# Performance work log

Measured on AMD Instinct MI355X. Metric: run time of the kernel, lower is better.

Reference implementation:

```python
import jax, jax.numpy as jnp
import numpy as np


def setup_inputs() -> dict:
    key = jax.random.key(0)
    B, C, H, W = 64, 128, 64, 64
    x = jax.random.normal(key, (B, C, H, W), dtype=jnp.float32)
    return {"x": x}


def reference(x) -> jnp.ndarray:
    # Covariance pooling: y = x_flat @ I_hat @ x_flat^T with
    # I_hat = (1/M) I - (1/M^2) ones(M,M).
    # Algebraically identical to (1/M) * (x - mean)(x - mean)^T, which
    # avoids materializing the MxM centering matrix.
    B, C, H, W = x.shape
    M = H * W
    xf = x.reshape(B, C, M)
    xc = xf - jnp.mean(xf, axis=2, keepdims=True)  # center over spatial dim
    y = jnp.einsum('bcm,bdm->bcd', xc, xc) / M     # [B, C, C]
    return y
```

## Files before the change

kernel.cpp:

```cpp
#include <hip/hip_runtime.h>

typedef __bf16 bf16x8 __attribute__((ext_vector_type(8)));
typedef float  f32x4  __attribute__((ext_vector_type(4)));
typedef unsigned short us8 __attribute__((ext_vector_type(8)));

#define B_      64
#define C_      128
#define M_      4096
#define KCHUNK  8
#define KC      (M_ / KCHUNK)
#define BK      64
#define NSLAB   (KC / BK)
#define LSTR    72

__device__ __forceinline__ unsigned short f2bf(float f) {
  unsigned u = __builtin_bit_cast(unsigned, f);
  u += 0x7fffu + ((u >> 16) & 1u);
  return (unsigned short)(u >> 16);
}
__device__ __forceinline__ float bf2f(unsigned short h) {
  unsigned u = ((unsigned)h) << 16;
  return __builtin_bit_cast(float, u);
}

__global__ __launch_bounds__(512, 4) void covpool_main(
    const float* __restrict__ x, unsigned short* __restrict__ Gp, float* __restrict__ Sp) {
  __shared__ unsigned short As[2][C_ * LSTR];

  const int tid  = threadIdx.x;
  const int b    = blockIdx.x >> 3;
  const int ch   = blockIdx.x & 7;

  const int row  = tid >> 3;
  const int col8 = tid & 7;

  const float* xp0 = x + ((size_t)(b * C_ + row) * M_) + (size_t)ch * KC + col8 * 8;
  const float* xp1 = xp0 + (size_t)64 * M_;

  const int lane = tid & 63;
  const int wave = tid >> 6;
  const int row0 = (wave >> 2) << 6;
  const int col0 = (wave & 3) << 5;
  const int lrow = lane & 15;
  const int quad = lane >> 4;

  f32x4 acc[4][2];
#pragma unroll
  for (int i = 0; i < 4; ++i)
#pragma unroll
    for (int j = 0; j < 2; ++j)
      acc[i][j] = (f32x4){0.f, 0.f, 0.f, 0.f};

  float sum0 = 0.f, sum1 = 0.f;

  float4 r0, r1, r2, r3;
  r0 = ((const float4*)xp0)[0]; r1 = ((const float4*)xp0)[1];
  r2 = ((const float4*)xp1)[0]; r3 = ((const float4*)xp1)[1];

#define STAGE(BUF)                                                                  \
  {                                                                                 \
    sum0 += (r0.x + r0.y) + (r0.z + r0.w) + (r1.x + r1.y) + (r1.z + r1.w);          \
    sum1 += (r2.x + r2.y) + (r2.z + r2.w) + (r3.x + r3.y) + (r3.z + r3.w);          \
    us8 v0 = { f2bf(r0.x), f2bf(r0.y), f2bf(r0.z), f2bf(r0.w),                      \
               f2bf(r1.x), f2bf(r1.y), f2bf(r1.z), f2bf(r1.w) };                    \
    us8 v1 = { f2bf(r2.x), f2bf(r2.y), f2bf(r2.z), f2bf(r2.w),                      \
               f2bf(r3.x), f2bf(r3.y), f2bf(r3.z), f2bf(r3.w) };                    \
    *(__shared__ us8*)&As[BUF][row * LSTR + col8 * 8]        = v0;                  \
    *(__shared__ us8*)&As[BUF][(64 + row) * LSTR + col8 * 8] = v1;                  \
  }

#define COMPUTE(BUF)                                                                \
  {                                                                                 \
    _Pragma("unroll")                                                               \
    for (int ks = 0; ks < 2; ++ks) {                                                \
      const int koff = ks * 32 + quad * 8;                                          \
      bf16x8 af[4], bfr[2];                                                         \
      _Pragma("unroll")                                                             \
      for (int i = 0; i < 4; ++i)                                                   \
        af[i] = *(const __shared__ bf16x8*)&As[BUF][(row0 + i * 16 + lrow) * LSTR + koff]; \
      _Pragma("unroll")                                                             \
      for (int j = 0; j < 2; ++j)                                                   \
        bfr[j] = *(const __shared__ bf16x8*)&As[BUF][(col0 + j * 16 + lrow) * LSTR + koff]; \
      _Pragma("unroll")                                                             \
      for (int i = 0; i < 4; ++i)                                                   \
        _Pragma("unroll")                                                           \
        for (int j = 0; j < 2; ++j)                                                 \
          acc[i][j] = __builtin_amdgcn_mfma_f32_16x16x32_bf16(af[i], bfr[j], acc[i][j], 0, 0, 0); \
    }                                                                               \
  }

#pragma unroll
  for (int s = 0; s < NSLAB; ++s) {
    STAGE(s & 1);
    __syncthreads();
    if (s + 1 < NSLAB) {
      const float* p0 = xp0 + (size_t)(s + 1) * BK;
      const float* p1 = xp1 + (size_t)(s + 1) * BK;
      r0 = ((const float4*)p0)[0]; r1 = ((const float4*)p0)[1];
      r2 = ((const float4*)p1)[0]; r3 = ((const float4*)p1)[1];
    }
    COMPUTE(s & 1);
  }

  unsigned short* gout = Gp + (((size_t)ch * B_ + b) << 14);
#pragma unroll
  for (int i = 0; i < 4; ++i)
#pragma unroll
    for (int j = 0; j < 2; ++j)
#pragma unroll
      for (int rr = 0; rr < 4; ++rr)
        gout[(size_t)(row0 + i * 16 + quad * 4 + rr) * C_ + (col0 + j * 16 + lrow)] =
            f2bf(acc[i][j][rr]);

  sum0 += __shfl_xor(sum0, 1); sum0 += __shfl_xor(sum0, 2); sum0 += __shfl_xor(sum0, 4);
  sum1 += __shfl_xor(sum1, 1); sum1 += __shfl_xor(sum1, 2); sum1 += __shfl_xor(sum1, 4);
  if ((tid & 7) == 0) {
    float* sout = Sp + (((size_t)ch * B_ + b) << 7);
    sout[row]      = sum0;
    sout[64 + row] = sum1;
  }
}

__global__ __launch_bounds__(256) void covpool_fix(
    const unsigned short* __restrict__ Gp, const float* __restrict__ Sp,
    float* __restrict__ y) {
  const int idx = (blockIdx.x * 256 + threadIdx.x) * 4;
  const int bb  = idx >> 14;
  const int rem = idx & 16383;
  const int cc  = rem >> 7;
  const int dd  = rem & 127;
  float g0 = 0.f, g1 = 0.f, g2 = 0.f, g3 = 0.f, sc = 0.f;
  float4 sd = {0.f, 0.f, 0.f, 0.f};
#pragma unroll
  for (int ch = 0; ch < KCHUNK; ++ch) {
    ushort4 gv = *(const ushort4*)&Gp[(((size_t)ch * B_ + bb) << 14) + rem];
    g0 += bf2f(gv.x); g1 += bf2f(gv.y); g2 += bf2f(gv.z); g3 += bf2f(gv.w);
    const float* sp = Sp + (((size_t)ch * B_ + bb) << 7);
    sc += sp[cc];
    float4 s4 = *(const float4*)&sp[dd];
    sd.x += s4.x; sd.y += s4.y; sd.z += s4.z; sd.w += s4.w;
  }
  const float invM = 1.f / (float)M_;
  const float scm = sc * invM;
  float4 out = { g0 * invM - scm * (sd.x * invM), g1 * invM - scm * (sd.y * invM),
                 g2 * invM - scm * (sd.z * invM), g3 * invM - scm * (sd.w * invM) };
  *(float4*)&y[idx] = out;
}

extern "C" void kernel_launch(void* const* d_in, const int* in_sizes, int n_in,
                              void* d_out, int out_size, void* d_ws, size_t ws_size,
                              hipStream_t stream) {
  const float* x = (const float*)d_in[0];
  float* out = (float*)d_out;
  unsigned short* wsG = (unsigned short*)d_ws;
  float* wsS = (float*)(wsG + (size_t)KCHUNK * B_ * C_ * C_);
  covpool_main<<<dim3(B_ * KCHUNK), dim3(512), 0, stream>>>(x, wsG, wsS);
  covpool_fix<<<dim3((B_ * C_ * C_) / 1024), dim3(256), 0, stream>>>(wsG, wsS, out);
}
```

Before: 197.1 us.

## Use larger single-buffered K slabs with batched per-row float4 loads

```diff
diff --git a/kernel.cpp b/kernel.cpp
--- a/kernel.cpp
+++ b/kernel.cpp
@@ -2,21 +2,20 @@
 
 typedef __bf16 bf16x8 __attribute__((ext_vector_type(8)));
 typedef float  f32x4  __attribute__((ext_vector_type(4)));
-typedef unsigned short us8 __attribute__((ext_vector_type(8)));
+typedef unsigned short us4 __attribute__((ext_vector_type(4)));
 
 #define B_      64
 #define C_      128
 #define M_      4096
 #define KCHUNK  8
 #define KC      (M_ / KCHUNK)
-#define BK      64
+#define BK      256
 #define NSLAB   (KC / BK)
-#define LSTR    72
+#define LSTR    264
 
 __device__ __forceinline__ unsigned short f2bf(float f) {
   unsigned u = __builtin_bit_cast(unsigned, f);
-  u += 0x7fffu + ((u >> 16) & 1u);
-  return (unsigned short)(u >> 16);
+  return (unsigned short)((u + 0x8000u) >> 16);
 }
 __device__ __forceinline__ float bf2f(unsigned short h) {
   unsigned u = ((unsigned)h) << 16;
@@ -25,20 +24,20 @@
 
 __global__ __launch_bounds__(512, 4) void covpool_main(
     const float* __restrict__ x, unsigned short* __restrict__ Gp, float* __restrict__ Sp) {
-  __shared__ unsigned short As[2][C_ * LSTR];
+  __shared__ unsigned short As[C_ * LSTR];
 
   const int tid  = threadIdx.x;
   const int b    = blockIdx.x >> 3;
   const int ch   = blockIdx.x & 7;
 
-  const int row  = tid >> 3;
-  const int col8 = tid & 7;
-
-  const float* xp0 = x + ((size_t)(b * C_ + row) * M_) + (size_t)ch * KC + col8 * 8;
-  const float* xp1 = xp0 + (size_t)64 * M_;
-
   const int lane = tid & 63;
   const int wave = tid >> 6;
+
+  const int lr   = lane >> 2;
+  const int q    = lane & 3;
+  const int row  = wave * 16 + lr;
+  const float* rowbase = x + ((size_t)(b * C_ + row) * M_) + (size_t)ch * KC;
+
   const int row0 = (wave >> 2) << 6;
   const int col0 = (wave & 3) << 5;
   const int lrow = lane & 15;
@@ -51,55 +50,48 @@
     for (int j = 0; j < 2; ++j)
       acc[i][j] = (f32x4){0.f, 0.f, 0.f, 0.f};
 
-  float sum0 = 0.f, sum1 = 0.f;
-
-  float4 r0, r1, r2, r3;
-  r0 = ((const float4*)xp0)[0]; r1 = ((const float4*)xp0)[1];
-  r2 = ((const float4*)xp1)[0]; r3 = ((const float4*)xp1)[1];
-
-#define STAGE(BUF)                                                                  \
-  {                                                                                 \
-    sum0 += (r0.x + r0.y) + (r0.z + r0.w) + (r1.x + r1.y) + (r1.z + r1.w);          \
-    sum1 += (r2.x + r2.y) + (r2.z + r2.w) + (r3.x + r3.y) + (r3.z + r3.w);          \
-    us8 v0 = { f2bf(r0.x), f2bf(r0.y), f2bf(r0.z), f2bf(r0.w),                      \
-               f2bf(r1.x), f2bf(r1.y), f2bf(r1.z), f2bf(r1.w) };                    \
-    us8 v1 = { f2bf(r2.x), f2bf(r2.y), f2bf(r2.z), f2bf(r2.w),                      \
-               f2bf(r3.x), f2bf(r3.y), f2bf(r3.z), f2bf(r3.w) };                    \
-    *(__shared__ us8*)&As[BUF][row * LSTR + col8 * 8]        = v0;                  \
-    *(__shared__ us8*)&As[BUF][(64 + row) * LSTR + col8 * 8] = v1;                  \
-  }
-
-#define COMPUTE(BUF)                                                                \
-  {                                                                                 \
-    _Pragma("unroll")                                                               \
-    for (int ks = 0; ks < 2; ++ks) {                                                \
-      const int koff = ks * 32 + quad * 8;                                          \
-      bf16x8 af[4], bfr[2];                                                         \
-      _Pragma("unroll")                                                             \
-      for (int i = 0; i < 4; ++i)                                                   \
-        af[i] = *(const __shared__ bf16x8*)&As[BUF][(row0 + i * 16 + lrow) * LSTR + koff]; \
-      _Pragma("unroll")                                                             \
-      for (int j = 0; j < 2; ++j)                                                   \
-        bfr[j] = *(const __shared__ bf16x8*)&As[BUF][(col0 + j * 16 + lrow) * LSTR + koff]; \
-      _Pragma("unroll")                                                             \
-      for (int i = 0; i < 4; ++i)                                                   \
-        _Pragma("unroll")                                                           \
-        for (int j = 0; j < 2; ++j)                                                 \
-          acc[i][j] = __builtin_amdgcn_mfma_f32_16x16x32_bf16(af[i], bfr[j], acc[i][j], 0, 0, 0); \
-    }                                                                               \
-  }
+  float sum = 0.f;
 
 #pragma unroll
   for (int s = 0; s < NSLAB; ++s) {
-    STAGE(s & 1);
+    const float4* rp = (const float4*)(rowbase + s * BK);
+    float4 L[8];
+#pragma unroll
+    for (int jj = 0; jj < 8; ++jj) L[jj] = rp[q + 4 * jj];
+#pragma unroll
+    for (int jj = 0; jj < 8; ++jj) {
+      float4 v = L[jj];
+      sum += (v.x + v.y) + (v.z + v.w);
+      us4 h = { f2bf(v.x), f2bf(v.y), f2bf(v.z), f2bf(v.w) };
+      *(__shared__ us4*)&As[row * LSTR + (q + 4 * jj) * 4] = h;
+    }
+#pragma unroll
+    for (int jj = 0; jj < 8; ++jj) L[jj] = rp[q + 4 * (8 + jj)];
+#pragma unroll
+    for (int jj = 0; jj < 8; ++jj) {
+      float4 v = L[jj];
+      sum += (v.x + v.y) + (v.z + v.w);
+      us4 h = { f2bf(v.x), f2bf(v.y), f2bf(v.z), f2bf(v.w) };
+      *(__shared__ us4*)&As[row * LSTR + (q + 4 * (8 + jj)) * 4] = h;
+    }
     __syncthreads();
-    if (s + 1 < NSLAB) {
-      const float* p0 = xp0 + (size_t)(s + 1) * BK;
-      const float* p1 = xp1 + (size_t)(s + 1) * BK;
-      r0 = ((const float4*)p0)[0]; r1 = ((const float4*)p0)[1];
-      r2 = ((const float4*)p1)[0]; r3 = ((const float4*)p1)[1];
+#pragma unroll
+    for (int ks = 0; ks < 8; ++ks) {
+      const int koff = ks * 32 + quad * 8;
+      bf16x8 af[4], bfr[2];
+#pragma unroll
+      for (int i = 0; i < 4; ++i)
+        af[i] = *(const __shared__ bf16x8*)&As[(row0 + i * 16 + lrow) * LSTR + koff];
+#pragma unroll
+      for (int j = 0; j < 2; ++j)
+        bfr[j] = *(const __shared__ bf16x8*)&As[(col0 + j * 16 + lrow) * LSTR + koff];
+#pragma unroll
+      for (int i = 0; i < 4; ++i)
+#pragma unroll
+        for (int j = 0; j < 2; ++j)
+          acc[i][j] = __builtin_amdgcn_mfma_f32_16x16x32_bf16(af[i], bfr[j], acc[i][j], 0, 0, 0);
     }
-    COMPUTE(s & 1);
+    __syncthreads();
   }
 
   unsigned short* gout = Gp + (((size_t)ch * B_ + b) << 14);
@@ -112,12 +104,10 @@
         gout[(size_t)(row0 + i * 16 + quad * 4 + rr) * C_ + (col0 + j * 16 + lrow)] =
             f2bf(acc[i][j][rr]);
 
-  sum0 += __shfl_xor(sum0, 1); sum0 += __shfl_xor(sum0, 2); sum0 += __shfl_xor(sum0, 4);
-  sum1 += __shfl_xor(sum1, 1); sum1 += __shfl_xor(sum1, 2); sum1 += __shfl_xor(sum1, 4);
-  if ((tid & 7) == 0) {
+  sum += __shfl_xor(sum, 1); sum += __shfl_xor(sum, 2);
+  if (q == 0) {
     float* sout = Sp + (((size_t)ch * B_ + b) << 7);
-    sout[row]      = sum0;
-    sout[64 + row] = sum1;
+    sout[row] = sum;
   }
 }
 
```

Result: no change. 199.8 us (+1.4%).
